# Kernel tuning notes

Measured on AMD Instinct MI355X. Metric: run time of the kernel, lower is better.

Reference implementation:

```python
import jax, jax.numpy as jnp
from jax import lax
import numpy as np

# ---- static configuration (RPN inference path) ----
B = 8
IMG_H, IMG_W = 800, 1216
LEVEL_GRIDS = [(200, 304), (100, 152), (50, 76), (25, 38), (13, 19)]
STRIDES = [4, 8, 16, 32, 64]
SIZES = [32, 64, 128, 256, 512]
RATIOS = np.array([0.5, 1.0, 2.0])
NUM_PER_LEVEL = [h * w * 3 for (h, w) in LEVEL_GRIDS]  # [182400,45600,11400,2850,741]
A_TOTAL = sum(NUM_PER_LEVEL)                            # 242991
PRE_N = 1000   # pre_nms_top_n['testing'], applied per level
POST_N = 1000  # post_nms_top_n['testing']
NMS_THRESH = 0.7
SCORE_THRESH = 0.0
MIN_SIZE = 0.001
BBOX_XFORM_CLIP = float(np.log(1000.0 / 16.0))
LEVEL_OFFSET = 4096.0  # > max image coord, for batched_nms level separation

K_PER_LEVEL = [min(PRE_N, n) for n in NUM_PER_LEVEL]
K_TOTAL = sum(K_PER_LEVEL)  # 4741
LEVELS = jnp.concatenate([jnp.full((k,), i, dtype=jnp.int32)
                          for i, k in enumerate(K_PER_LEVEL)])


def _make_anchors():
    """torchvision-style grid anchors, one scale + 3 aspect ratios per level."""
    all_anchors = []
    for (fh, fw), stride, size in zip(LEVEL_GRIDS, STRIDES, SIZES):
        h_ratios = np.sqrt(RATIOS)
        w_ratios = 1.0 / h_ratios
        ws = w_ratios * size
        hs = h_ratios * size
        base = np.stack([-ws / 2, -hs / 2, ws / 2, hs / 2], axis=1)  # [3,4]
        sx = np.arange(fw, dtype=np.float32) * stride
        sy = np.arange(fh, dtype=np.float32) * stride
        yy, xx = np.meshgrid(sy, sx, indexing='ij')
        shifts = np.stack([xx, yy, xx, yy], axis=-1).reshape(-1, 1, 4)  # [fh*fw,1,4]
        anchors = (shifts + base[None]).reshape(-1, 4)                  # [fh*fw*3,4]
        all_anchors.append(anchors.astype(np.float32))
    return np.concatenate(all_anchors, axis=0)  # [A_TOTAL,4]


def setup_inputs() -> dict:
    key = jax.random.key(0)
    k1, k2 = jax.random.split(key)
    objectness = jax.random.normal(k1, (B, A_TOTAL), dtype=jnp.float32)
    pred_bbox_deltas = jax.random.normal(k2, (B, A_TOTAL, 4), dtype=jnp.float32) * 0.5
    anchors = jnp.asarray(_make_anchors())
    return {"objectness": objectness, "pred_bbox_deltas": pred_bbox_deltas,
            "anchors": anchors}


def _decode(deltas, anchors):
    """BoxCoder.decode with weights (1,1,1,1). deltas [B,A,4], anchors [A,4]."""
    wa = anchors[:, 2] - anchors[:, 0]
    ha = anchors[:, 3] - anchors[:, 1]
    cxa = anchors[:, 0] + 0.5 * wa
    cya = anchors[:, 1] + 0.5 * ha
    dx, dy, dw, dh = deltas[..., 0], deltas[..., 1], deltas[..., 2], deltas[..., 3]
    dw = jnp.minimum(dw, BBOX_XFORM_CLIP)
    dh = jnp.minimum(dh, BBOX_XFORM_CLIP)
    cx = dx * wa + cxa
    cy = dy * ha + cya
    w = jnp.exp(dw) * wa
    h = jnp.exp(dh) * ha
    return jnp.stack([cx - 0.5 * w, cy - 0.5 * h, cx + 0.5 * w, cy + 0.5 * h], axis=-1)


def _per_level_topk(objectness):
    """_get_top_n_idx: per-level top-k with global offsets. Returns [B,K_TOTAL] int32."""
    idxs, offset = [], 0
    for n, k in zip(NUM_PER_LEVEL, K_PER_LEVEL):
        _, ti = lax.top_k(objectness[:, offset:offset + n], k)
        idxs.append(ti + offset)
        offset += n
    return jnp.concatenate(idxs, axis=1)


def _iou(boxes):  # boxes [K,4] -> [K,K]
    area = (boxes[:, 2] - boxes[:, 0]) * (boxes[:, 3] - boxes[:, 1])
    lt = jnp.maximum(boxes[:, None, :2], boxes[None, :, :2])
    rb = jnp.minimum(boxes[:, None, 2:], boxes[None, :, 2:])
    wh = jnp.clip(rb - lt, 0.0)
    inter = wh[..., 0] * wh[..., 1]
    return inter / (area[:, None] + area[None, :] - inter)


def _nms_image(boxes, scores, levels, valid):
    """clip->filter->batched_nms->post_nms_top_n for one image (fixed shapes)."""
    K = boxes.shape[0]
    order = jnp.argsort(-jnp.where(valid, scores, -jnp.inf))
    b = boxes[order]
    s = scores[order]
    v = valid[order]
    lv = levels[order]
    # batched NMS: offset boxes by level so cross-level boxes never overlap
    bb = b + lv.astype(b.dtype)[:, None] * LEVEL_OFFSET
    iou = lax.stop_gradient(_iou(bb))  # keep decisions are non-differentiable
    idxr = jnp.arange(K)

    def body(i, keep):
        sup = (iou[i] > NMS_THRESH) & (idxr > i) & keep[i]
        return keep & ~sup

    keep = lax.fori_loop(0, K, body, v)
    sel = jnp.where(keep, s, -1.0)  # sigmoid scores are > 0
    top_s, top_i = lax.top_k(sel, POST_N)
    kept = top_s > 0.0
    out_b = jnp.where(kept[:, None], b[top_i], 0.0)
    out_s = jnp.where(kept, top_s, 0.0)
    return out_b, out_s


def reference(objectness, pred_bbox_deltas, anchors):
    # box decode for all anchors
    proposals = _decode(pred_bbox_deltas, anchors)          # [B,A,4]
    # per-level topk + gather
    idx = _per_level_topk(objectness)                       # [B,K]
    obj = jnp.take_along_axis(objectness, idx, axis=1)      # [B,K]
    props = jnp.take_along_axis(proposals, idx[..., None], axis=1)  # [B,K,4]
    scores = jax.nn.sigmoid(obj)
    lv = jnp.broadcast_to(LEVELS, idx.shape)
    # clip_boxes_to_image
    x1 = jnp.clip(props[..., 0], 0.0, IMG_W)
    y1 = jnp.clip(props[..., 1], 0.0, IMG_H)
    x2 = jnp.clip(props[..., 2], 0.0, IMG_W)
    y2 = jnp.clip(props[..., 3], 0.0, IMG_H)
    props = jnp.stack([x1, y1, x2, y2], axis=-1)
    # remove_small_boxes + score_thresh
    valid = (x2 - x1 >= MIN_SIZE) & (y2 - y1 >= MIN_SIZE) & (scores >= SCORE_THRESH)
    boxes_out, scores_out = jax.vmap(_nms_image)(props, scores, lv, valid)
    return boxes_out, scores_out  # [B,POST_N,4], [B,POST_N] (zero-padded)
```

## Files before the change

### kernel.cpp

```cpp
#include <hip/hip_runtime.h>
#include <stdint.h>

#pragma clang fp contract(off)

typedef unsigned int u32;
typedef unsigned long long u64;

#define A_TOTAL 242991
#define KTOT    4741

__constant__ int c_LN[5]   = {182400, 45600, 11400, 2850, 741};
__constant__ int c_LOFF[5] = {0, 182400, 228000, 239400, 242250};
__constant__ int c_LK[5]   = {1000, 1000, 1000, 1000, 741};

__constant__ int c_SL[33] = {0,0,0,0,0,0,0,0,0,0,0,0,0,0,0,0,0,0,0,0,0,0,0,
                             1,1,1,1,1,1, 2,2, 3, 4};
__constant__ int c_SS[33] = {0,8192,16384,24576,32768,40960,49152,57344,65536,
                             73728,81920,90112,98304,106496,114688,122880,131072,
                             139264,147456,155648,163840,172032,180224,
                             0,8192,16384,24576,32768,40960, 0,8192, 0, 0};

__constant__ int c_MW[40] = {0,1,2,3, 4,4, 5,5, 6,6, 7,7, 8,8,8, 9,9,9,
                             10,10,10, 11,11,11, 12,12,12,12, 13,13,13,13,
                             14,14,14,14, 15,15,15,15};
__constant__ int c_MR[40] = {0,0,0,0, 0,1, 0,1, 0,1, 0,1, 0,1,2, 0,1,2,
                             0,1,2, 0,1,2, 0,1,2,3, 0,1,2,3,
                             0,1,2,3, 0,1,2,3};

static const size_t OFF_KEEPW    = 0;
static const size_t OFF_HIST     = 0;
static const size_t OFF_SELCNT   = 327680;
static const size_t OFF_CANDCNT  = 327840;
static const size_t MEMSET_BYTES = 328000;
static const size_t OFF_TBIN     = 328000;
static const size_t OFF_CLESS    = 328160;
static const size_t OFF_SELG     = 328320;
static const size_t OFF_CANDG    = 656000;
static const size_t OFF_KEYS     = 1966720;
static const size_t OFF_BOX      = 2270144;
static const size_t OFF_SCORE    = 2876992;
static const size_t OFF_VALID    = 3028704;
static const size_t OFF_MASK     = 3180416;
static const size_t OFF_OUTK     = 8423296;

__device__ __forceinline__ u32 fmap(float f){
  u32 b = __float_as_uint(f);
  return (b & 0x80000000u) ? ~b : (b | 0x80000000u);
}
__device__ __forceinline__ float funmap(u32 m){
  return __uint_as_float((m & 0x80000000u) ? (m & 0x7FFFFFFFu) : ~m);
}

__global__ void __launch_bounds__(1024)
k_hist(const float* __restrict__ obj, u32* __restrict__ hist)
{
  int b = blockIdx.x / 33, s = blockIdx.x % 33;
  int l = c_SL[s], start = c_SS[s];
  int cnt = c_LN[l] - start; if (cnt > 8192) cnt = 8192;
  int bl = b * 5 + l;
  __shared__ u32 h[4][2048];
  for (int i = threadIdx.x; i < 8192; i += 1024) ((u32*)h)[i] = 0;
  __syncthreads();
  u32* hw = h[(threadIdx.x >> 6) & 3];
  const float* p = obj + (size_t)b * A_TOTAL + c_LOFF[l] + start;
  int head = (4 - (int)(((size_t)p >> 2) & 3)) & 3;
  if (head > cnt) head = cnt;
  if ((int)threadIdx.x < head) atomicAdd(&hw[(~fmap(p[threadIdx.x])) >> 21], 1u);
  int nvec = (cnt - head) >> 2;
  const float4* pv = (const float4*)(p + head);
  for (int i = threadIdx.x; i < nvec; i += 1024){
    float4 v = pv[i];
    atomicAdd(&hw[(~fmap(v.x)) >> 21], 1u);
    atomicAdd(&hw[(~fmap(v.y)) >> 21], 1u);
    atomicAdd(&hw[(~fmap(v.z)) >> 21], 1u);
    atomicAdd(&hw[(~fmap(v.w)) >> 21], 1u);
  }
  int tail0 = head + (nvec << 2);
  int ntail = cnt - tail0;
  if ((int)threadIdx.x < ntail) atomicAdd(&hw[(~fmap(p[tail0 + threadIdx.x])) >> 21], 1u);
  __syncthreads();
  for (int i = threadIdx.x; i < 2048; i += 1024){
    u32 v = h[0][i] + h[1][i] + h[2][i] + h[3][i];
    if (v) atomicAdd(&hist[bl * 2048 + i], v);
  }
}

__global__ void __launch_bounds__(256)
k_cutoff(u32* __restrict__ hist, u32* __restrict__ tbin, u32* __restrict__ cless)
{
  int bl = blockIdx.x; int l = bl % 5;
  int K = c_LK[l], n = c_LN[l];
  int tid = threadIdx.x;
  __shared__ u32 cum[2048];
  __shared__ u32 part[256];
  __shared__ int s_t;
  u32 vals[8]; u32 sum = 0;
  for (int q = 0; q < 8; ++q){ vals[q] = hist[bl * 2048 + tid * 8 + q]; sum += vals[q]; }
  part[tid] = sum;
  __syncthreads();
  for (int off = 1; off < 256; off <<= 1){
    u32 add = (tid >= off) ? part[tid - off] : 0u;
    __syncthreads();
    part[tid] += add;
    __syncthreads();
  }
  u32 run = (tid > 0) ? part[tid - 1] : 0u;
  for (int q = 0; q < 8; ++q){ run += vals[q]; cum[tid * 8 + q] = run; }
  __syncthreads();
  for (int q = 0; q < 8; ++q) hist[bl * 2048 + tid * 8 + q] = cum[tid * 8 + q];
  if (K >= n){ if (tid == 0){ tbin[bl] = 2048u; cless[bl] = (u32)n; } return; }
  if (tid == 0) s_t = 0;
  __syncthreads();
  for (int q = 0; q < 8; ++q){
    int i = tid * 8 + q;
    u32 c = cum[i], cp = (i > 0) ? cum[i - 1] : 0u;
    if (c >= (u32)K && cp < (u32)K) s_t = i;
  }
  __syncthreads();
  if (tid == 0){
    int t = s_t;
    tbin[bl] = (u32)t;
    cless[bl] = (t > 0) ? cum[t - 1] : 0u;
  }
}

#define SELCAP 2048
#define CANDCAP 1024
__global__ void __launch_bounds__(1024)
k_collect(const float* __restrict__ obj, const u32* __restrict__ tbin,
          u32* __restrict__ selcnt, u32* __restrict__ candcnt,
          u64* __restrict__ selg, u64* __restrict__ candg)
{
  int b = blockIdx.x / 33, s = blockIdx.x % 33;
  int l = c_SL[s], start = c_SS[s];
  int cnt = c_LN[l] - start; if (cnt > 8192) cnt = 8192;
  int bl = b * 5 + l;
  u32 t = tbin[bl];
  __shared__ u64 lsel[SELCAP];
  __shared__ u64 lcand[CANDCAP];
  __shared__ u32 lcs, lcc, gbs, gbc;
  if (threadIdx.x == 0){ lcs = 0u; lcc = 0u; }
  __syncthreads();
  const float* p = obj + (size_t)b * A_TOTAL + c_LOFF[l] + start;

  auto push = [&](u32 m, int idx){
    u32 bin = m >> 21;
    u64 key = ((u64)m << 32) | (u32)idx;
    if (bin < t){
      u32 pos = atomicAdd(&lcs, 1u);
      if (pos < SELCAP) lsel[pos] = key;
      else { u32 gp = atomicAdd(&selcnt[bl], 1u); selg[(size_t)bl * 1024 + gp] = key; }
    } else if (bin == t){
      u32 pos = atomicAdd(&lcc, 1u);
      if (pos < CANDCAP) lcand[pos] = key;
      else { u32 gp = atomicAdd(&candcnt[bl], 1u); if (gp < 4096u) candg[(size_t)bl * 4096 + gp] = key; }
    }
  };

  int head = (4 - (int)(((size_t)p >> 2) & 3)) & 3;
  if (head > cnt) head = cnt;
  if ((int)threadIdx.x < head) push(~fmap(p[threadIdx.x]), start + (int)threadIdx.x);
  int nvec = (cnt - head) >> 2;
  const float4* pv = (const float4*)(p + head);
  for (int i = threadIdx.x; i < nvec; i += 1024){
    float4 v = pv[i];
    int e = start + head + (i << 2);
    push(~fmap(v.x), e);
    push(~fmap(v.y), e + 1);
    push(~fmap(v.z), e + 2);
    push(~fmap(v.w), e + 3);
  }
  int tail0 = head + (nvec << 2);
  int ntail = cnt - tail0;
  if ((int)threadIdx.x < ntail) push(~fmap(p[tail0 + threadIdx.x]), start + tail0 + (int)threadIdx.x);
  __syncthreads();
  u32 ns = lcs;  if (ns > SELCAP) ns = SELCAP;
  u32 ncd = lcc; if (ncd > CANDCAP) ncd = CANDCAP;
  if (threadIdx.x == 0){
    gbs = ns  ? atomicAdd(&selcnt[bl],  ns)  : 0u;
    gbc = ncd ? atomicAdd(&candcnt[bl], ncd) : 0u;
  }
  __syncthreads();
  u32 bs = gbs, bc = gbc;
  for (u32 i = threadIdx.x; i < ns; i += 1024)
    selg[(size_t)bl * 1024 + bs + i] = lsel[i];
  for (u32 i = threadIdx.x; i < ncd; i += 1024){
    u32 gp = bc + i;
    if (gp < 4096u) candg[(size_t)bl * 4096 + gp] = lcand[i];
  }
}

__global__ void __launch_bounds__(1024)
k_select(const u32* __restrict__ selcnt, const u32* __restrict__ candcnt,
         const u64* __restrict__ selg, const u64* __restrict__ candg,
         const u32* __restrict__ cum_g, u64* __restrict__ keys)
{
  int bl = blockIdx.x; int b = bl / 5, l = bl % 5;
  int K = c_LK[l];
  int tid = threadIdx.x;
  __shared__ u32 cumL[2048];
  __shared__ u32 cnt[2048];
  __shared__ u32 part[256];
  __shared__ u64 selU[1024];
  __shared__ u64 candU[4096];
  for (int i = tid; i < 2048; i += 1024){ cumL[i] = cum_g[bl * 2048 + i]; cnt[i] = 0u; }
  __syncthreads();
  u32 ns = selcnt[bl]; if (ns > 1024u) ns = 1024u;
  u32 nc = candcnt[bl]; if (nc > 4096u) nc = 4096u;
  int R = K - (int)ns;
  u64* kout = keys + (size_t)b * KTOT + l * 1000;
  if (tid < (int)ns){
    u64 key = selg[(size_t)bl * 1024 + tid];
    u32 bin = (u32)(key >> 53);
    u32 lo = bin ? cumL[bin - 1] : 0u;
    u32 a = atomicAdd(&cnt[bin], 1u);
    selU[lo + a] = key;
  }
  __syncthreads();
  if (tid < (int)ns){
    u64 key = selU[tid];
    u32 bin = (u32)(key >> 53);
    u32 lo = bin ? cumL[bin - 1] : 0u;
    u32 hi = cumL[bin];
    u32 r = 0;
    for (u32 j = lo; j < hi; ++j) r += (selU[j] < key) ? 1u : 0u;
    kout[lo + r] = key;
  }
  if (R > 0){
    __syncthreads();
    for (int i = tid; i < 2048; i += 1024) cnt[i] = 0u;
    __syncthreads();
    for (u32 i = tid; i < nc; i += 1024){
      u64 key = candg[(size_t)bl * 4096 + i];
      atomicAdd(&cnt[(u32)(key >> 42) & 2047u], 1u);
    }
    __syncthreads();
    u32 vals[8]; u32 sum = 0;
    if (tid < 256){
      for (int q = 0; q < 8; ++q){ vals[q] = cnt[tid * 8 + q]; sum += vals[q]; }
      part[tid] = sum;
    }
    __syncthreads();
    for (int off = 1; off < 256; off <<= 1){
      u32 add = (tid < 256 && tid >= off) ? part[tid - off] : 0u;
      __syncthreads();
      if (tid < 256) part[tid] += add;
      __syncthreads();
    }
    if (tid < 256){
      u32 run = tid ? part[tid - 1] : 0u;
      for (int q = 0; q < 8; ++q){ run += vals[q]; cnt[tid * 8 + q] = run; }
    }
    __syncthreads();
    u32* arr2 = (u32*)selU;
    for (int i = tid; i < 2048; i += 1024) arr2[i] = 0u;
    __syncthreads();
    for (u32 i = tid; i < nc; i += 1024){
      u64 key = candg[(size_t)bl * 4096 + i];
      u32 sb = (u32)(key >> 42) & 2047u;
      u32 lo = sb ? cnt[sb - 1] : 0u;
      u32 a = atomicAdd(&arr2[sb], 1u);
      candU[lo + a] = key;
    }
    __syncthreads();
    for (u32 s = tid; s < nc; s += 1024){
      u64 key = candU[s];
      u32 sb = (u32)(key >> 42) & 2047u;
      u32 lo = sb ? cnt[sb - 1] : 0u;
      u32 hi = cnt[sb];
      u32 r = 0;
      for (u32 j = lo; j < hi; ++j) r += (candU[j] < key) ? 1u : 0u;
      u32 pos = lo + r;
      if (pos < (u32)R) kout[ns + pos] = key;
    }
  }
}

__global__ void __launch_bounds__(256)
k_decode(const u64* __restrict__ keys, const float* __restrict__ deltas,
         const float* __restrict__ anchors, float* __restrict__ boxes,
         float* __restrict__ scores, u32* __restrict__ valid)
{
  int g = blockIdx.x * 256 + threadIdx.x;
  if (g >= 8 * KTOT) return;
  int b = g / KTOT, kpos = g % KTOT;
  int l = kpos / 1000; if (l > 4) l = 4;
  u64 key = keys[g];
  u32 idx = (u32)key;
  float o = funmap(~(u32)(key >> 32));
  int ai = c_LOFF[l] + (int)idx;
  const float* a = anchors + (size_t)ai * 4;
  const float* d = deltas + ((size_t)b * A_TOTAL + ai) * 4;
  float a0 = a[0], a1 = a[1], a2 = a[2], a3 = a[3];
  float wa = __fsub_rn(a2, a0), ha = __fsub_rn(a3, a1);
  float cxa = __fadd_rn(a0, __fmul_rn(0.5f, wa));
  float cya = __fadd_rn(a1, __fmul_rn(0.5f, ha));
  float dx = d[0], dy = d[1];
  float dw = fminf(d[2], 4.135166556742356f);
  float dh = fminf(d[3], 4.135166556742356f);
  float cx = __fadd_rn(__fmul_rn(dx, wa), cxa);
  float cy = __fadd_rn(__fmul_rn(dy, ha), cya);
  float w  = __fmul_rn(expf(dw), wa);
  float h  = __fmul_rn(expf(dh), ha);
  float hw = __fmul_rn(0.5f, w), hh = __fmul_rn(0.5f, h);
  float x1 = __fsub_rn(cx, hw), y1 = __fsub_rn(cy, hh);
  float x2 = __fadd_rn(cx, hw), y2 = __fadd_rn(cy, hh);
  x1 = fminf(fmaxf(x1, 0.0f), 1216.0f);
  x2 = fminf(fmaxf(x2, 0.0f), 1216.0f);
  y1 = fminf(fmaxf(y1, 0.0f), 800.0f);
  y2 = fminf(fmaxf(y2, 0.0f), 800.0f);
  float s = __fdiv_rn(1.0f, __fadd_rn(1.0f, expf(-o)));
  int v = (__fsub_rn(x2, x1) >= 0.001f) && (__fsub_rn(y2, y1) >= 0.001f) && (s >= 0.0f);
  float* bo = boxes + (size_t)g * 4;
  bo[0] = x1; bo[1] = y1; bo[2] = x2; bo[3] = y2;
  scores[g] = s;
  valid[g] = (u32)v;
}

__global__ void __launch_bounds__(256)
k_mask(const float* __restrict__ boxes, u64* __restrict__ mask)
{
  int b = blockIdx.x / 184, s = blockIdx.x % 184;
  int l, idx;
  if (s < 160){ l = s / 40; idx = s % 40; }
  else        { l = 4;      idx = s - 160; }
  int w = c_MW[idx], rb = c_MR[idx];
  int N = c_LK[l];
  int koff = l * 1000;
  float offv = (float)(l * 4096);
  __shared__ float sjx1[64], sjy1[64], sjx2[64], sjy2[64], sjar[64];
  int jbase = w * 64;
  if (threadIdx.x < 64){
    int j = jbase + (int)threadIdx.x;
    float x1, y1, x2, y2, ar;
    if (j < N){
      float4 p = ((const float4*)boxes)[(size_t)(b * KTOT + koff + j)];
      x1 = __fadd_rn(p.x, offv); y1 = __fadd_rn(p.y, offv);
      x2 = __fadd_rn(p.z, offv); y2 = __fadd_rn(p.w, offv);
      ar = __fmul_rn(__fsub_rn(x2, x1), __fsub_rn(y2, y1));
    } else {
      x1 = 3e38f; y1 = 3e38f; x2 = -3e38f; y2 = -3e38f; ar = 0.f;
    }
    sjx1[threadIdx.x] = x1; sjy1[threadIdx.x] = y1;
    sjx2[threadIdx.x] = x2; sjy2[threadIdx.x] = y2; sjar[threadIdx.x] = ar;
  }
  __syncthreads();
  int i = rb * 256 + (int)threadIdx.x;
  int rows = (w + 1) * 64; if (rows > N) rows = N;
  if (i >= rows) return;
  float4 p = ((const float4*)boxes)[(size_t)(b * KTOT + koff + i)];
  float bx1 = __fadd_rn(p.x, offv), by1 = __fadd_rn(p.y, offv);
  float bx2 = __fadd_rn(p.z, offv), by2 = __fadd_rn(p.w, offv);
  float bar = __fmul_rn(__fsub_rn(bx2, bx1), __fsub_rn(by2, by1));
  u64 bw = 0;
  #pragma unroll 16
  for (int jj = 0; jj < 64; ++jj){
    int j = jbase + jj;
    float ltx = fmaxf(bx1, sjx1[jj]), lty = fmaxf(by1, sjy1[jj]);
    float rbx = fminf(bx2, sjx2[jj]), rby = fminf(by2, sjy2[jj]);
    float wx = fmaxf(__fsub_rn(rbx, ltx), 0.0f);
    float wy = fmaxf(__fsub_rn(rby, lty), 0.0f);
    float inter = __fmul_rn(wx, wy);
    bool sup = false;
    if (inter > 0.0f && j > i){
      float den = __fsub_rn(__fadd_rn(bar, sjar[jj]), inter);
      sup = __fdiv_rn(inter, den) > 0.7f;
    }
    bw |= ((u64)sup) << jj;
  }
  mask[((size_t)(b * 5 + l) * 16 + w) * 1024 + i] = bw;
}

__global__ void __launch_bounds__(256)
k_nms(const u64* __restrict__ mask, const u32* __restrict__ valid,
      const float* __restrict__ scores, u64* __restrict__ outk,
      u64* __restrict__ keepw)
{
  int bl = blockIdx.x; int b = bl / 5, l = bl % 5;
  int N = c_LK[l], koff = l * 1000;
  int WN = (N + 63) >> 6;
  int tid = threadIdx.x;
  __shared__ u64 s_kw[16];
  __shared__ u64 s_m[7680];
  const u64* mb = mask + (size_t)bl * 16 * 1024;
  int wstage = (WN < 15) ? WN : 15;
  for (int w = 0; w < wstage; ++w){
    int rows = (w + 1) * 64;
    int base = 32 * w * (w + 1);
    for (int r = tid; r < rows; r += 256)
      s_m[base + r] = mb[(size_t)w * 1024 + r];
  }
  __syncthreads();
  if (tid < 64){
    int lane = tid;
    for (int c = 0; c < WN; ++c){
      int i = c * 64 + lane;
      int pred = (i < N) && (valid[(size_t)b * KTOT + koff + i] != 0u);
      u64 bal = __ballot(pred);
      if (lane == 0) s_kw[c] = bal;
    }
    for (int w = 0; w < WN; ++w){
      u64 kwv = s_kw[w];
      u64 supl = 0;
      if (w < 15){
        int base = 32 * w * (w + 1);
        for (int jb = 0; jb < w; ++jb){
          u64 kb = s_kw[jb];
          u64 m = s_m[base + jb * 64 + lane];
          supl |= (((kb >> lane) & 1ULL) ? m : 0ULL);
        }
      } else {
        for (int jb = 0; jb < w; ++jb){
          u64 kb = s_kw[jb];
          u64 m = mb[(size_t)w * 1024 + jb * 64 + lane];
          supl |= (((kb >> lane) & 1ULL) ? m : 0ULL);
        }
      }
      int jr = w * 64 + lane;
      u64 rowl;
      if (w < 15) rowl = s_m[32 * w * (w + 1) + jr];
      else        rowl = (jr < N) ? mb[(size_t)w * 1024 + jr] : 0ULL;
      bool inC = ((kwv >> lane) & 1ULL) != 0ULL;
      u64 rkw = rowl & kwv;
      u64 confl = inC ? rkw : 0ULL;
      u32 a0 = (u32)supl, a1 = (u32)(supl >> 32);
      u32 a2 = (u32)confl, a3 = (u32)(confl >> 32);
      for (int off = 32; off; off >>= 1){
        a0 |= __shfl_xor(a0, off);
        a1 |= __shfl_xor(a1, off);
        a2 |= __shfl_xor(a2, off);
        a3 |= __shfl_xor(a3, off);
      }
      supl = ((u64)a1 << 32) | a0;
      u64 conf = ((u64)a3 << 32) | a2;
      u64 srcb = __ballot(inC && (rkw != 0ULL));
      u64 cur = kwv & ~supl;
      u64 kept = cur;
      if (((srcb & cur) != 0ULL) && ((conf & cur) != 0ULL)){
        u32 rowl_lo = (u32)rowl, rowl_hi = (u32)(rowl >> 32);
        u64 act = cur & (srcb | conf);
        while (act){
          int ib  = __ffsll((unsigned long long)act) - 1;
          int ibs = __builtin_amdgcn_readfirstlane(ib);
          u64 bit = 1ULL << ibs;
          act &= ~bit;
          if (kept & bit){
            u32 rlo = (u32)__builtin_amdgcn_readlane((int)rowl_lo, ibs);
            u32 rhi = (u32)__builtin_amdgcn_readlane((int)rowl_hi, ibs);
            u64 r   = ((u64)rhi << 32) | rlo;
            kept &= ~r;
            act  &= ~r;
          }
        }
      }
      if (lane == 0) s_kw[w] = kept;
    }
  }
  __syncthreads();
  if (tid < 16) keepw[(size_t)bl * 16 + tid] = (tid < WN) ? s_kw[tid] : 0ULL;
  for (int i = tid; i < N; i += 256){
    u64 key = ~0ULL;
    if ((s_kw[i >> 6] >> (i & 63)) & 1ULL){
      float sc = scores[(size_t)b * KTOT + koff + i];
      key = ((u64)(~fmap(sc)) << 32) | (u32)(koff + i);
    }
    outk[(size_t)b * KTOT + koff + i] = key;
  }
}

#define CMPN 1024
__global__ void __launch_bounds__(256)
k_rank(const u64* __restrict__ outk, const u64* __restrict__ keepw,
       const float* __restrict__ boxes, float* __restrict__ out)
{
  int b = blockIdx.x / 19, chunk = blockIdx.x % 19;
  int tid = threadIdx.x;
  __shared__ u64 cmp[5 * CMPN];
  __shared__ u64 kw[80];
  for (int i = tid; i < 5 * CMPN; i += 256) cmp[i] = ~0ULL;
  if (tid < 80) kw[tid] = keepw[(size_t)b * 80 + tid];
  __syncthreads();
  for (int i = tid; i < KTOT; i += 256){
    u64 key = outk[(size_t)b * KTOT + i];
    if (key != ~0ULL){
      int l = i / 1000; if (l > 4) l = 4;
      int li = i - l * 1000;
      int wi = li >> 6, bit = li & 63;
      const u64* kwl = &kw[l * 16];
      int r = __popcll(kwl[wi] & ((1ULL << bit) - 1ULL));
      for (int w = 0; w < wi; ++w) r += __popcll(kwl[w]);
      cmp[l * CMPN + r] = key;
    }
  }
  __syncthreads();
  int i = chunk * 256 + tid;
  if (i >= KTOT) return;
  u64 key = outk[(size_t)b * KTOT + i];
  if (key == ~0ULL) return;
  int l = i / 1000; if (l > 4) l = 4;
  int li = i - l * 1000;
  int wi = li >> 6, bit = li & 63;
  const u64* kwl = &kw[l * 16];
  int rank = __popcll(kwl[wi] & ((1ULL << bit) - 1ULL));
  for (int w = 0; w < wi; ++w) rank += __popcll(kwl[w]);
  #pragma unroll
  for (int lo = 0; lo < 5; ++lo){
    if (lo == l) continue;
    int pos = 0;
    #pragma unroll
    for (int s = 512; s > 0; s >>= 1)
      if (cmp[lo * CMPN + pos + s - 1] < key) pos += s;
    rank += pos;
  }
  if (rank < 1000){
    float4 bx = ((const float4*)boxes)[(size_t)(b * KTOT + i)];
    ((float4*)out)[(size_t)(b * 1000 + rank)] = bx;
    out[32000 + b * 1000 + rank] = funmap(~(u32)(key >> 32));
  }
}

extern "C" void kernel_launch(void* const* d_in, const int* in_sizes, int n_in,
                              void* d_out, int out_size, void* d_ws, size_t ws_size,
                              hipStream_t stream)
{
  (void)in_sizes; (void)n_in; (void)ws_size;
  const float* obj     = (const float*)d_in[0];
  const float* deltas  = (const float*)d_in[1];
  const float* anchors = (const float*)d_in[2];
  float* out = (float*)d_out;
  char* ws = (char*)d_ws;

  u32* hist    = (u32*)(ws + OFF_HIST);
  u64* keepw   = (u64*)(ws + OFF_KEEPW);
  u32* selcnt  = (u32*)(ws + OFF_SELCNT);
  u32* candcnt = (u32*)(ws + OFF_CANDCNT);
  u32* tbin    = (u32*)(ws + OFF_TBIN);
  u32* cless   = (u32*)(ws + OFF_CLESS);
  u64* selg    = (u64*)(ws + OFF_SELG);
  u64* candg   = (u64*)(ws + OFF_CANDG);
  u64* keys    = (u64*)(ws + OFF_KEYS);
  float* boxes = (float*)(ws + OFF_BOX);
  float* score = (float*)(ws + OFF_SCORE);
  u32* valid   = (u32*)(ws + OFF_VALID);
  u64* mask    = (u64*)(ws + OFF_MASK);
  u64* outk    = (u64*)(ws + OFF_OUTK);

  hipMemsetAsync(ws, 0, MEMSET_BYTES, stream);
  hipMemsetAsync(d_out, 0, (size_t)out_size * sizeof(float), stream);
  hipLaunchKernelGGL(k_hist,    dim3(264),  dim3(1024), 0, stream, obj, hist);
  hipLaunchKernelGGL(k_cutoff,  dim3(40),   dim3(256),  0, stream, hist, tbin, cless);
  hipLaunchKernelGGL(k_collect, dim3(264),  dim3(1024), 0, stream, obj, tbin, selcnt, candcnt, selg, candg);
  hipLaunchKernelGGL(k_select,  dim3(40),   dim3(1024), 0, stream, selcnt, candcnt, selg, candg, hist, keys);
  hipLaunchKernelGGL(k_decode,  dim3(149),  dim3(256),  0, stream, keys, deltas, anchors, boxes, score, valid);
  hipLaunchKernelGGL(k_mask,    dim3(1472), dim3(256),  0, stream, boxes, mask);
  hipLaunchKernelGGL(k_nms,     dim3(40),   dim3(256),  0, stream, mask, valid, score, outk, keepw);
  hipLaunchKernelGGL(k_rank,    dim3(152),  dim3(256),  0, stream, outk, keepw, boxes, out);
}
```

Baseline: 142.8 us.

## Replace bucketed rank-sort in k_select with brute-force all-pairs rank counting

```diff
diff --git a/kernel.cpp b/kernel.cpp
--- a/kernel.cpp
+++ b/kernel.cpp
@@ -107,7 +107,6 @@
   u32 run = (tid > 0) ? part[tid - 1] : 0u;
   for (int q = 0; q < 8; ++q){ run += vals[q]; cum[tid * 8 + q] = run; }
   __syncthreads();
-  for (int q = 0; q < 8; ++q) hist[bl * 2048 + tid * 8 + q] = cum[tid * 8 + q];
   if (K >= n){ if (tid == 0){ tbin[bl] = 2048u; cless[bl] = (u32)n; } return; }
   if (tid == 0) s_t = 0;
   __syncthreads();
@@ -193,85 +192,42 @@
 __global__ void __launch_bounds__(1024)
 k_select(const u32* __restrict__ selcnt, const u32* __restrict__ candcnt,
          const u64* __restrict__ selg, const u64* __restrict__ candg,
-         const u32* __restrict__ cum_g, u64* __restrict__ keys)
+         u64* __restrict__ keys)
 {
   int bl = blockIdx.x; int b = bl / 5, l = bl % 5;
   int K = c_LK[l];
   int tid = threadIdx.x;
-  __shared__ u32 cumL[2048];
-  __shared__ u32 cnt[2048];
-  __shared__ u32 part[256];
-  __shared__ u64 selU[1024];
-  __shared__ u64 candU[4096];
-  for (int i = tid; i < 2048; i += 1024){ cumL[i] = cum_g[bl * 2048 + i]; cnt[i] = 0u; }
-  __syncthreads();
+  __shared__ __align__(16) u64 selU[1024];
+  __shared__ __align__(16) u64 candU[4098];
   u32 ns = selcnt[bl]; if (ns > 1024u) ns = 1024u;
   u32 nc = candcnt[bl]; if (nc > 4096u) nc = 4096u;
   int R = K - (int)ns;
+  selU[tid] = (tid < (int)ns) ? selg[(size_t)bl * 1024 + tid] : ~0ULL;
+  for (u32 i = tid; i < nc; i += 1024) candU[i] = candg[(size_t)bl * 4096 + i];
+  u32 nce = (nc + 1u) & ~1u;
+  if (tid == 0 && nce > nc) candU[nc] = ~0ULL;
+  __syncthreads();
   u64* kout = keys + (size_t)b * KTOT + l * 1000;
   if (tid < (int)ns){
-    u64 key = selg[(size_t)bl * 1024 + tid];
-    u32 bin = (u32)(key >> 53);
-    u32 lo = bin ? cumL[bin - 1] : 0u;
-    u32 a = atomicAdd(&cnt[bin], 1u);
-    selU[lo + a] = key;
-  }
-  __syncthreads();
-  if (tid < (int)ns){
     u64 key = selU[tid];
-    u32 bin = (u32)(key >> 53);
-    u32 lo = bin ? cumL[bin - 1] : 0u;
-    u32 hi = cumL[bin];
     u32 r = 0;
-    for (u32 j = lo; j < hi; ++j) r += (selU[j] < key) ? 1u : 0u;
-    kout[lo + r] = key;
+    #pragma unroll 8
+    for (u32 j = 0; j < 1024; j += 2){
+      ulonglong2 v = *reinterpret_cast<const ulonglong2*>(&selU[j]);
+      r += (v.x < key) + (v.y < key);
+    }
+    kout[r] = key;
   }
   if (R > 0){
-    __syncthreads();
-    for (int i = tid; i < 2048; i += 1024) cnt[i] = 0u;
-    __syncthreads();
-    for (u32 i = tid; i < nc; i += 1024){
-      u64 key = candg[(size_t)bl * 4096 + i];
-      atomicAdd(&cnt[(u32)(key >> 42) & 2047u], 1u);
-    }
-    __syncthreads();
-    u32 vals[8]; u32 sum = 0;
-    if (tid < 256){
-      for (int q = 0; q < 8; ++q){ vals[q] = cnt[tid * 8 + q]; sum += vals[q]; }
-      part[tid] = sum;
-    }
-    __syncthreads();
-    for (int off = 1; off < 256; off <<= 1){
-      u32 add = (tid < 256 && tid >= off) ? part[tid - off] : 0u;
-      __syncthreads();
-      if (tid < 256) part[tid] += add;
-      __syncthreads();
-    }
-    if (tid < 256){
-      u32 run = tid ? part[tid - 1] : 0u;
-      for (int q = 0; q < 8; ++q){ run += vals[q]; cnt[tid * 8 + q] = run; }
-    }
-    __syncthreads();
-    u32* arr2 = (u32*)selU;
-    for (int i = tid; i < 2048; i += 1024) arr2[i] = 0u;
-    __syncthreads();
-    for (u32 i = tid; i < nc; i += 1024){
-      u64 key = candg[(size_t)bl * 4096 + i];
-      u32 sb = (u32)(key >> 42) & 2047u;
-      u32 lo = sb ? cnt[sb - 1] : 0u;
-      u32 a = atomicAdd(&arr2[sb], 1u);
-      candU[lo + a] = key;
-    }
-    __syncthreads();
     for (u32 s = tid; s < nc; s += 1024){
       u64 key = candU[s];
-      u32 sb = (u32)(key >> 42) & 2047u;
-      u32 lo = sb ? cnt[sb - 1] : 0u;
-      u32 hi = cnt[sb];
       u32 r = 0;
-      for (u32 j = lo; j < hi; ++j) r += (candU[j] < key) ? 1u : 0u;
-      u32 pos = lo + r;
-      if (pos < (u32)R) kout[ns + pos] = key;
+      #pragma unroll 8
+      for (u32 j = 0; j < nce; j += 2){
+        ulonglong2 v = *reinterpret_cast<const ulonglong2*>(&candU[j]);
+        r += (v.x < key) + (v.y < key);
+      }
+      if (r < (u32)R) kout[ns + r] = key;
     }
   }
 }
@@ -550,7 +506,7 @@
   hipLaunchKernelGGL(k_hist,    dim3(264),  dim3(1024), 0, stream, obj, hist);
   hipLaunchKernelGGL(k_cutoff,  dim3(40),   dim3(256),  0, stream, hist, tbin, cless);
   hipLaunchKernelGGL(k_collect, dim3(264),  dim3(1024), 0, stream, obj, tbin, selcnt, candcnt, selg, candg);
-  hipLaunchKernelGGL(k_select,  dim3(40),   dim3(1024), 0, stream, selcnt, candcnt, selg, candg, hist, keys);
+  hipLaunchKernelGGL(k_select,  dim3(40),   dim3(1024), 0, stream, selcnt, candcnt, selg, candg, keys);
   hipLaunchKernelGGL(k_decode,  dim3(149),  dim3(256),  0, stream, keys, deltas, anchors, boxes, score, valid);
   hipLaunchKernelGGL(k_mask,    dim3(1472), dim3(256),  0, stream, boxes, mask);
   hipLaunchKernelGGL(k_nms,     dim3(40),   dim3(256),  0, stream, mask, valid, score, outk, keepw);
```

Measured after the change: 131.4 us. 1.09x faster.
